# Performance work log

Hardware: AMD Instinct MI355X
Metric: run time of the kernel (lower is better)

## Reference

```python
import jax, jax.numpy as jnp
import numpy as np

N_NODES = 100000
N_EDGES = 1600000
D = 128            # in_channels == hidden_channels
N_CLASSES = 10
N_GRAPHS = 512
N_CONVS = 3        # num_layers - 1


def _linear_params(key, d_in, d_out):
    kw, kb = jax.random.split(key)
    bound = 1.0 / np.sqrt(d_in)
    w = jax.random.uniform(kw, (d_in, d_out), jnp.float32, -bound, bound)
    b = jax.random.uniform(kb, (d_out,), jnp.float32, -bound, bound)
    return w, b


def setup_inputs() -> dict:
    key = jax.random.key(0)
    ks = jax.random.split(key, 16)
    x = jax.random.normal(ks[0], (N_NODES, D), jnp.float32)
    edge_index = jax.random.randint(ks[1], (2, N_EDGES), 0, N_NODES, jnp.int64)
    batch = jnp.sort(jax.random.randint(ks[2], (N_NODES,), 0, N_GRAPHS, jnp.int64))
    inp = {"x": x, "edge_index": edge_index, "batch": batch}
    # 3 GIN convs, each an MLP: Linear(D,D) -> ReLU -> Linear(D,D)
    for i in range(N_CONVS):
        w1, b1 = _linear_params(ks[3 + 2 * i], D, D)
        w2, b2 = _linear_params(ks[4 + 2 * i], D, D)
        inp[f"w1_{i}"], inp[f"b1_{i}"] = w1, b1
        inp[f"w2_{i}"], inp[f"b2_{i}"] = w2, b2
    wl, bl = _linear_params(ks[10], D, N_CLASSES)
    inp["w_lin"], inp["b_lin"] = wl, bl
    return inp


def _gin_conv(x, src, dst, w1, b1, w2, b2):
    # sum_{j->i} x_j  (scatter-add over edges), eps = 0 (PyG default)
    agg = jax.ops.segment_sum(x[src], dst, num_segments=N_NODES)
    h = agg + x  # (1 + eps) * x + aggregate
    h = jax.nn.relu(h @ w1 + b1) @ w2 + b2  # nn.Sequential MLP
    return h


def reference(x, edge_index, batch,
              w1_0, b1_0, w2_0, b2_0,
              w1_1, b1_1, w2_1, b2_1,
              w1_2, b1_2, w2_2, b2_2,
              w_lin, b_lin):
    src, dst = edge_index[0], edge_index[1]
    params = [(w1_0, b1_0, w2_0, b2_0),
              (w1_1, b1_1, w2_1, b2_1),
              (w1_2, b1_2, w2_2, b2_2)]
    for (w1, b1, w2, b2) in params:
        x = _gin_conv(x, src, dst, w1, b1, w2, b2)
        x = jax.nn.relu(x)
    pooled = jax.ops.segment_sum(x, batch, num_segments=N_GRAPHS)  # global_add_pool
    return pooled @ w_lin + b_lin
```

## Files before the change

### kernel.cpp

```cpp
#include <hip/hip_runtime.h>
#include <hip/hip_bf16.h>

#define N_NODES 100000
#define N_EDGES 1600000
#define DIM 128
#define N_GRAPHS 512
#define N_CLASSES 10
#define SCAN_CHUNK 1024

#define NBK 782
#define EB 8192
#define NEB 196
#define HN (NBK * NEB)
#define NCH_HIST ((HN + SCAN_CHUNK - 1) / SCAN_CHUNK)

#define POOL_CHUNK 128
#define NPB ((N_NODES + POOL_CHUNK - 1) / POOL_CHUNK)

typedef __attribute__((ext_vector_type(8))) short short8;
typedef __attribute__((ext_vector_type(4))) float floatx4;

__device__ __forceinline__ uint bfround(float f) {
    uint u = __builtin_bit_cast(uint, f);
    return (u + 0x7fffu + ((u >> 16) & 1u)) >> 16;
}
__device__ __forceinline__ float bflo(uint u) { return __builtin_bit_cast(float, u << 16); }
__device__ __forceinline__ float bfhi(uint u) { return __builtin_bit_cast(float, u & 0xffff0000u); }

__device__ __forceinline__ void addrow(float* a, uint4 v) {
    a[0] += bflo(v.x); a[1] += bfhi(v.x);
    a[2] += bflo(v.y); a[3] += bfhi(v.y);
    a[4] += bflo(v.z); a[5] += bfhi(v.z);
    a[6] += bflo(v.w); a[7] += bfhi(v.w);
}

struct WPtrs { const float* w[6]; };

__global__ void k_cvt_x(const float* __restrict__ x, ushort* __restrict__ xb,
                        WPtrs wp, ushort* __restrict__ wt) {
    int stride = gridDim.x * blockDim.x;
    int t0 = blockIdx.x * blockDim.x + threadIdx.x;
    for (int i = t0; i < N_NODES * DIM / 4; i += stride) {
        floatx4 v = *(const floatx4*)(x + (size_t)i * 4);
        ushort4 o;
        o.x = (ushort)bfround(v.x);
        o.y = (ushort)bfround(v.y);
        o.z = (ushort)bfround(v.z);
        o.w = (ushort)bfround(v.w);
        *(ushort4*)(xb + (size_t)i * 4) = o;
    }
    for (int j = t0; j < 6 * 16384; j += stride) {
        int m = j >> 14, idx = j & 16383;
        int n = idx >> 7, k = idx & 127;
        wt[j] = (ushort)bfround(wp.w[m][k * 128 + n]);
    }
}


__global__ __launch_bounds__(256) void k_hist(const int* __restrict__ dstv,
                                              int* __restrict__ hist,
                                              float* __restrict__ pooled) {
    int gt = blockIdx.x * 256 + threadIdx.x;
    for (int i = gt; i < N_GRAPHS * DIM; i += NEB * 256) pooled[i] = 0.f;

    __shared__ int cnt[NBK];
    int blk = blockIdx.x, tid = threadIdx.x;
    for (int i = tid; i < NBK; i += 256) cnt[i] = 0;
    __syncthreads();
    int base = blk * EB;
    int end = min(base + EB, N_EDGES);
    for (int i = base + tid; i < end; i += 256) atomicAdd(&cnt[dstv[i] >> 7], 1);
    __syncthreads();
    for (int b = tid; b < NBK; b += 256) hist[b * NEB + blk] = cnt[b];
}

__global__ __launch_bounds__(256) void k_reduce(const int* __restrict__ src, int n,
                                                int* __restrict__ chunk_sums) {
    int base = blockIdx.x * SCAN_CHUNK;
    int tid = threadIdx.x;
    int s = 0;
    for (int i = tid; i < SCAN_CHUNK; i += 256) {
        int idx = base + i;
        if (idx < n) s += src[idx];
    }
    __shared__ int red[256];
    red[tid] = s;
    __syncthreads();
    for (int off = 128; off > 0; off >>= 1) {
        if (tid < off) red[tid] += red[tid + off];
        __syncthreads();
    }
    if (tid == 0) chunk_sums[blockIdx.x] = red[0];
}

__global__ __launch_bounds__(256) void k_scan_c(int* __restrict__ chunk_sums, int nch) {
    __shared__ int sm[256];
    int tid = threadIdx.x;
    int v = (tid < nch) ? chunk_sums[tid] : 0;
    sm[tid] = v;
    __syncthreads();
    for (int off = 1; off < 256; off <<= 1) {
        int t = (tid >= off) ? sm[tid - off] : 0;
        __syncthreads();
        sm[tid] += t;
        __syncthreads();
    }
    if (tid < nch) chunk_sums[tid] = sm[tid] - v;
}

__global__ __launch_bounds__(256) void k_apply(const int* __restrict__ src,
                                               const int* __restrict__ chunk_sums,
                                               int* __restrict__ dst, int n) {
    int base = blockIdx.x * SCAN_CHUNK;
    int tid = threadIdx.x;
    int i0 = base + tid * 4;
    int v[4];
    int s = 0;
    #pragma unroll
    for (int j = 0; j < 4; j++) {
        int idx = i0 + j;
        v[j] = (idx < n) ? src[idx] : 0;
        s += v[j];
    }
    __shared__ int sc[256];
    sc[tid] = s;
    __syncthreads();
    for (int off = 1; off < 256; off <<= 1) {
        int t = (tid >= off) ? sc[tid - off] : 0;
        __syncthreads();
        sc[tid] += t;
        __syncthreads();
    }
    int excl = sc[tid] - s + chunk_sums[blockIdx.x];
    #pragma unroll
    for (int j = 0; j < 4; j++) {
        int idx = i0 + j;
        if (idx < n) dst[idx] = excl;
        excl += v[j];
    }
}

__global__ __launch_bounds__(256) void k_scatter(const int* __restrict__ srcv,
                                                 const int* __restrict__ dstv,
                                                 const int* __restrict__ hists,
                                                 uint* __restrict__ sorted) {
    __shared__ int cur[NBK];
    int blk = blockIdx.x, tid = threadIdx.x;
    for (int b = tid; b < NBK; b += 256) cur[b] = hists[b * NEB + blk];
    __syncthreads();
    int base = blk * EB;
    int end = min(base + EB, N_EDGES);
    for (int i = base + tid; i < end; i += 256) {
        int s = srcv[i], d = dstv[i];
        int p = atomicAdd(&cur[d >> 7], 1);
        sorted[p] = (uint)s | ((uint)(d & 127) << 17);
    }
}

__global__ __launch_bounds__(256) void k_build(const int* __restrict__ hists,
                                               const uint* __restrict__ sorted,
                                               int* __restrict__ row_ptr,
                                               int* __restrict__ col) {
    __shared__ int cnt[128];
    __shared__ int scn[128];
    __shared__ int cur[128];
    int b = blockIdx.x, tid = threadIdx.x;
    if (tid < 128) cnt[tid] = 0;
    __syncthreads();
    int s0 = hists[b * NEB];
    int s1 = (b == NBK - 1) ? N_EDGES : hists[(b + 1) * NEB];
    for (int i = s0 + tid; i < s1; i += 256) atomicAdd(&cnt[(sorted[i] >> 17) & 127], 1);
    __syncthreads();
    if (tid < 128) scn[tid] = cnt[tid];
    __syncthreads();
    for (int off = 1; off < 128; off <<= 1) {
        int t = (tid < 128 && tid >= off) ? scn[tid - off] : 0;
        __syncthreads();
        if (tid < 128) scn[tid] += t;
        __syncthreads();
    }
    int node = (b << 7) + tid;
    if (tid < 128) {
        int excl = s0 + scn[tid] - cnt[tid];
        cur[tid] = excl;
        if (node < N_NODES) row_ptr[node] = excl;
    }
    if (b == 0 && tid == 0) row_ptr[N_NODES] = N_EDGES;
    __syncthreads();
    for (int i = s0 + tid; i < s1; i += 256) {
        uint e = sorted[i];
        int p = atomicAdd(&cur[(e >> 17) & 127], 1);
        col[p] = (int)(e & 0x1FFFFu);
    }
}

__global__ __launch_bounds__(256) void k_agg(const uint4* __restrict__ xr,
                                             const int* __restrict__ row_ptr,
                                             const int* __restrict__ col,
                                             uint4* __restrict__ hr) {
    int wv = threadIdx.x >> 6;
    int nA = blockIdx.x * 8 + wv * 2;
    if (nA >= N_NODES) return;
    int nB = nA + 1;
    bool hasB = nB < N_NODES;
    int lane = threadIdx.x & 63;
    int grp = lane >> 4;
    int l16 = lane & 15;

    float accA[8], accB[8];
    #pragma unroll
    for (int i = 0; i < 8; i++) { accA[i] = 0.f; accB[i] = 0.f; }
    if (grp == 0) {
        uint4 sv = xr[(size_t)nA * 16 + l16];
        accA[0] = bflo(sv.x); accA[1] = bfhi(sv.x);
        accA[2] = bflo(sv.y); accA[3] = bfhi(sv.y);
        accA[4] = bflo(sv.z); accA[5] = bfhi(sv.z);
        accA[6] = bflo(sv.w); accA[7] = bfhi(sv.w);
    } else if (grp == 1 && hasB) {
        uint4 sv = xr[(size_t)nB * 16 + l16];
        accB[0] = bflo(sv.x); accB[1] = bfhi(sv.x);
        accB[2] = bflo(sv.y); accB[3] = bfhi(sv.y);
        accB[4] = bflo(sv.z); accB[5] = bfhi(sv.z);
        accB[6] = bflo(sv.w); accB[7] = bfhi(sv.w);
    }

    int jA = row_ptr[nA], eA = row_ptr[nA + 1];
    int jB = hasB ? row_ptr[nB] : 0;
    int eB = hasB ? row_ptr[nB + 1] : 0;

    while (jA < eA || jB < eB) {
        int chunkA = eA - jA; chunkA = chunkA < 0 ? 0 : (chunkA > 64 ? 64 : chunkA);
        int chunkB = eB - jB; chunkB = chunkB < 0 ? 0 : (chunkB > 64 ? 64 : chunkB);
        int myA = (lane < chunkA) ? col[jA + lane] : 0;
        int myB = (lane < chunkB) ? col[jB + lane] : 0;
        int cm = chunkA > chunkB ? chunkA : chunkB;
        int iters = (cm + 15) >> 4;
        for (int f = 0; f < iters; f++) {
            int p = (f << 4) + grp;
            int a0 = __shfl(myA, (p      < chunkA) ? p      : 0);
            int a1 = __shfl(myA, (p + 4  < chunkA) ? p + 4  : 0);
            int a2 = __shfl(myA, (p + 8  < chunkA) ? p + 8  : 0);
            int a3 = __shfl(myA, (p + 12 < chunkA) ? p + 12 : 0);
            int b0 = __shfl(myB, (p      < chunkB) ? p      : 0);
            int b1 = __shfl(myB, (p + 4  < chunkB) ? p + 4  : 0);
            int b2 = __shfl(myB, (p + 8  < chunkB) ? p + 8  : 0);
            int b3 = __shfl(myB, (p + 12 < chunkB) ? p + 12 : 0);
            uint4 vA0 = xr[(size_t)a0 * 16 + l16];
            uint4 vA1 = xr[(size_t)a1 * 16 + l16];
            uint4 vA2 = xr[(size_t)a2 * 16 + l16];
            uint4 vA3 = xr[(size_t)a3 * 16 + l16];
            uint4 vB0 = xr[(size_t)b0 * 16 + l16];
            uint4 vB1 = xr[(size_t)b1 * 16 + l16];
            uint4 vB2 = xr[(size_t)b2 * 16 + l16];
            uint4 vB3 = xr[(size_t)b3 * 16 + l16];
            if (p < chunkA)      addrow(accA, vA0);
            if (p + 4 < chunkA)  addrow(accA, vA1);
            if (p + 8 < chunkA)  addrow(accA, vA2);
            if (p + 12 < chunkA) addrow(accA, vA3);
            if (p < chunkB)      addrow(accB, vB0);
            if (p + 4 < chunkB)  addrow(accB, vB1);
            if (p + 8 < chunkB)  addrow(accB, vB2);
            if (p + 12 < chunkB) addrow(accB, vB3);
        }
        jA += 64; jB += 64;
    }

    #pragma unroll
    for (int i = 0; i < 8; i++) {
        accA[i] += __shfl_xor(accA[i], 16);
        accA[i] += __shfl_xor(accA[i], 32);
        accB[i] += __shfl_xor(accB[i], 16);
        accB[i] += __shfl_xor(accB[i], 32);
    }

    if (grp == 0) {
        uint4 o;
        o.x = bfround(accA[0]) | (bfround(accA[1]) << 16);
        o.y = bfround(accA[2]) | (bfround(accA[3]) << 16);
        o.z = bfround(accA[4]) | (bfround(accA[5]) << 16);
        o.w = bfround(accA[6]) | (bfround(accA[7]) << 16);
        hr[(size_t)nA * 16 + l16] = o;
    } else if (grp == 1 && hasB) {
        uint4 o;
        o.x = bfround(accB[0]) | (bfround(accB[1]) << 16);
        o.y = bfround(accB[2]) | (bfround(accB[3]) << 16);
        o.z = bfround(accB[4]) | (bfround(accB[5]) << 16);
        o.w = bfround(accB[6]) | (bfround(accB[7]) << 16);
        hr[(size_t)nB * 16 + l16] = o;
    }
}

__device__ __forceinline__ int loff(int row, int byte) {
    return row * 256 + (byte ^ ((row & 7) << 4));
}

__global__ __launch_bounds__(256) void k_mlp(const ushort* __restrict__ hin,
                                             ushort* __restrict__ xout,
                                             const ushort* __restrict__ W1t,
                                             const float* __restrict__ b1,
                                             const ushort* __restrict__ W2t,
                                             const float* __restrict__ b2) {
    __shared__ alignas(16) char hT[64 * 256];
    int tid = threadIdx.x;
    int lane = tid & 63;
    int wave = tid >> 6;
    int node0 = blockIdx.x * 64;
    int l15 = lane & 15;
    int lhi = lane >> 4;
    int ncol0 = wave * 32;

    #pragma unroll
    for (int it = 0; it < 4; ++it) {
        int idx = it * 256 + tid;
        int row = idx >> 4;
        int cb = (idx & 15) * 16;
        int gn = node0 + row;
        floatx4 v = {0.f, 0.f, 0.f, 0.f};
        if (gn < N_NODES) v = *(const floatx4*)(hin + (size_t)gn * 128 + cb / 2);
        *(floatx4*)(hT + loff(row, cb)) = v;
    }
    __syncthreads();

    short8 bf[4][2];
    #pragma unroll
    for (int ks = 0; ks < 4; ks++)
        #pragma unroll
        for (int nf = 0; nf < 2; nf++) {
            int nrow = ncol0 + nf * 16 + l15;
            bf[ks][nf] = *(const short8*)(W1t + nrow * 128 + ks * 32 + lhi * 8);
        }

    floatx4 acc[4][2];
    #pragma unroll
    for (int m = 0; m < 4; m++)
        #pragma unroll
        for (int nf = 0; nf < 2; nf++) {
            float bias = b1[ncol0 + nf * 16 + l15];
            acc[m][nf] = (floatx4){bias, bias, bias, bias};
        }

    #pragma unroll
    for (int ks = 0; ks < 4; ks++) {
        short8 af[4];
        #pragma unroll
        for (int m = 0; m < 4; m++)
            af[m] = *(const short8*)(hT + loff(m * 16 + l15, ks * 64 + lhi * 16));
        #pragma unroll
        for (int m = 0; m < 4; m++)
            #pragma unroll
            for (int nf = 0; nf < 2; nf++)
                acc[m][nf] = __builtin_amdgcn_mfma_f32_16x16x32_bf16(af[m], bf[ks][nf], acc[m][nf], 0, 0, 0);
    }
    __syncthreads();

    #pragma unroll
    for (int m = 0; m < 4; m++)
        #pragma unroll
        for (int nf = 0; nf < 2; nf++) {
            int colb = (ncol0 + nf * 16 + l15) * 2;
            #pragma unroll
            for (int j = 0; j < 4; j++) {
                int row = m * 16 + lhi * 4 + j;
                float t = acc[m][nf][j];
                t = t > 0.f ? t : 0.f;
                *(ushort*)(hT + loff(row, colb)) = (ushort)bfround(t);
            }
        }
    __syncthreads();

    #pragma unroll
    for (int ks = 0; ks < 4; ks++)
        #pragma unroll
        for (int nf = 0; nf < 2; nf++) {
            int nrow = ncol0 + nf * 16 + l15;
            bf[ks][nf] = *(const short8*)(W2t + nrow * 128 + ks * 32 + lhi * 8);
        }
    #pragma unroll
    for (int m = 0; m < 4; m++)
        #pragma unroll
        for (int nf = 0; nf < 2; nf++) {
            float bias = b2[ncol0 + nf * 16 + l15];
            acc[m][nf] = (floatx4){bias, bias, bias, bias};
        }

    #pragma unroll
    for (int ks = 0; ks < 4; ks++) {
        short8 af[4];
        #pragma unroll
        for (int m = 0; m < 4; m++)
            af[m] = *(const short8*)(hT + loff(m * 16 + l15, ks * 64 + lhi * 16));
        #pragma unroll
        for (int m = 0; m < 4; m++)
            #pragma unroll
            for (int nf = 0; nf < 2; nf++)
                acc[m][nf] = __builtin_amdgcn_mfma_f32_16x16x32_bf16(af[m], bf[ks][nf], acc[m][nf], 0, 0, 0);
    }
    __syncthreads();

    #pragma unroll
    for (int m = 0; m < 4; m++)
        #pragma unroll
        for (int nf = 0; nf < 2; nf++) {
            int colb = (ncol0 + nf * 16 + l15) * 2;
            #pragma unroll
            for (int j = 0; j < 4; j++) {
                int row = m * 16 + lhi * 4 + j;
                float t = acc[m][nf][j];
                t = t > 0.f ? t : 0.f;
                *(ushort*)(hT + loff(row, colb)) = (ushort)bfround(t);
            }
        }
    __syncthreads();
    #pragma unroll
    for (int it = 0; it < 4; ++it) {
        int idx = it * 256 + tid;
        int row = idx >> 4;
        int cb = (idx & 15) * 16;
        int gn = node0 + row;
        if (gn < N_NODES)
            *(floatx4*)(xout + (size_t)gn * 128 + cb / 2) = *(const floatx4*)(hT + loff(row, cb));
    }
}

__global__ __launch_bounds__(256) void k_pool(const uint* __restrict__ x,
                                              const int* __restrict__ batch,
                                              float* __restrict__ pooled) {
    int n0 = blockIdx.x * POOL_CHUNK;
    int wave = threadIdx.x >> 6;
    int lane = threadIdx.x & 63;
    float a0 = 0.f, a1 = 0.f;
    int cur = -1;
    int endn = min(n0 + POOL_CHUNK, N_NODES);
    for (int n = n0 + wave; n < endn; n += 4) {
        int g = batch[n];
        if (g != cur) {
            if (cur >= 0) {
                atomicAdd(&pooled[cur * 128 + lane * 2], a0);
                atomicAdd(&pooled[cur * 128 + lane * 2 + 1], a1);
            }
            cur = g; a0 = 0.f; a1 = 0.f;
        }
        uint v = x[(size_t)n * 64 + lane];
        a0 += bflo(v); a1 += bfhi(v);
    }
    if (cur >= 0) {
        atomicAdd(&pooled[cur * 128 + lane * 2], a0);
        atomicAdd(&pooled[cur * 128 + lane * 2 + 1], a1);
    }
}

__global__ __launch_bounds__(64) void k_final(const float* __restrict__ pooled,
                                              const float* __restrict__ wl,
                                              const float* __restrict__ bl,
                                              float* __restrict__ out) {
    int g = blockIdx.x;
    int o = threadIdx.x;
    if (o >= N_CLASSES) return;
    float acc = bl[o];
    for (int k = 0; k < 128; k++) acc += pooled[g * 128 + k] * wl[k * N_CLASSES + o];
    out[g * N_CLASSES + o] = acc;
}


extern "C" void kernel_launch(void* const* d_in, const int* in_sizes, int n_in,
                              void* d_out, int out_size, void* d_ws, size_t ws_size,
                              hipStream_t stream) {
    const float* x0  = (const float*)d_in[0];
    const int* ei    = (const int*)d_in[1];
    const int* batch = (const int*)d_in[2];
    const float* W1[3] = {(const float*)d_in[3], (const float*)d_in[7],  (const float*)d_in[11]};
    const float* B1[3] = {(const float*)d_in[4], (const float*)d_in[8],  (const float*)d_in[12]};
    const float* W2[3] = {(const float*)d_in[5], (const float*)d_in[9],  (const float*)d_in[13]};
    const float* B2[3] = {(const float*)d_in[6], (const float*)d_in[10], (const float*)d_in[14]};
    const float* wl = (const float*)d_in[15];
    const float* bl = (const float*)d_in[16];
    float* out = (float*)d_out;

    const int* srcv = ei;
    const int* dstv = ei + N_EDGES;

    char* w = (char*)d_ws;
    ushort* xb = (ushort*)w;
    ushort* hb = xb + (size_t)N_NODES * DIM;
    ushort* wt = hb + (size_t)N_NODES * DIM;
    float* pooled = (float*)(wt + 6 * 128 * 128);
    int* row_ptr = (int*)(pooled + N_GRAPHS * DIM);
    int* colidx  = row_ptr + (N_NODES + 2);
    int* chunk_sums = colidx + N_EDGES;
    int* hist    = chunk_sums + 256;
    uint* sorted = (uint*)(hist + HN + 1);

    WPtrs wp;
    wp.w[0] = W1[0]; wp.w[1] = W2[0]; wp.w[2] = W1[1];
    wp.w[3] = W2[1]; wp.w[4] = W1[2]; wp.w[5] = W2[2];
    hipLaunchKernelGGL(k_cvt_x, dim3(2048), dim3(256), 0, stream, x0, xb, wp, wt);

    hipLaunchKernelGGL(k_hist, dim3(NEB), dim3(256), 0, stream, dstv, hist, pooled);
    hipLaunchKernelGGL(k_reduce, dim3(NCH_HIST), dim3(256), 0, stream, hist, HN, chunk_sums);
    hipLaunchKernelGGL(k_scan_c, dim3(1), dim3(256), 0, stream, chunk_sums, NCH_HIST);
    hipLaunchKernelGGL(k_apply, dim3(NCH_HIST), dim3(256), 0, stream, hist, chunk_sums, hist, HN);
    hipLaunchKernelGGL(k_scatter, dim3(NEB), dim3(256), 0, stream, srcv, dstv, hist, sorted);
    hipLaunchKernelGGL(k_build, dim3(NBK), dim3(256), 0, stream, hist, sorted, row_ptr, colidx);

    dim3 aggGrid((N_NODES + 7) / 8), aggBlk(256);
    dim3 mlpGrid((N_NODES + 63) / 64), mlpBlk(256);
    for (int l = 0; l < 3; l++) {
        hipLaunchKernelGGL(k_agg, aggGrid, aggBlk, 0, stream,
                           (const uint4*)xb, row_ptr, colidx, (uint4*)hb);
        hipLaunchKernelGGL(k_mlp, mlpGrid, mlpBlk, 0, stream,
                           hb, xb, wt + (size_t)(2 * l) * 16384, B1[l],
                           wt + (size_t)(2 * l + 1) * 16384, B2[l]);
    }

    hipLaunchKernelGGL(k_pool, dim3(NPB), dim3(256), 0, stream, (const uint*)xb, batch, pooled);
    hipLaunchKernelGGL(k_final, dim3(N_GRAPHS), dim3(64), 0, stream, pooled, wl, bl, out);
}
```

Before: 330.6 us.

## Fuse conversion with histogram, fold chunk scan into apply, pool inside MLP

Merges the input/weight bf16 conversion kernel with the edge histogram kernel by splitting blocks by role. Removes the single-block chunk-scan kernel by having each apply block reduce the preceding chunk sums itself. Fuses global add pooling into the last MLP layer, reading results from shared memory instead of re-reading from global. This cuts three kernel launches and one pass over the node features, at the cost of redundant prefix reductions per block and extra atomics in the MLP kernel.

```diff
diff --git a/kernel.cpp b/kernel.cpp
--- a/kernel.cpp
+++ b/kernel.cpp
@@ -14,9 +14,6 @@
 #define HN (NBK * NEB)
 #define NCH_HIST ((HN + SCAN_CHUNK - 1) / SCAN_CHUNK)
 
-#define POOL_CHUNK 128
-#define NPB ((N_NODES + POOL_CHUNK - 1) / POOL_CHUNK)
-
 typedef __attribute__((ext_vector_type(8))) short short8;
 typedef __attribute__((ext_vector_type(4))) float floatx4;
 
@@ -36,42 +33,43 @@
 
 struct WPtrs { const float* w[6]; };
 
-__global__ void k_cvt_x(const float* __restrict__ x, ushort* __restrict__ xb,
-                        WPtrs wp, ushort* __restrict__ wt) {
-    int stride = gridDim.x * blockDim.x;
-    int t0 = blockIdx.x * blockDim.x + threadIdx.x;
-    for (int i = t0; i < N_NODES * DIM / 4; i += stride) {
-        floatx4 v = *(const floatx4*)(x + (size_t)i * 4);
-        ushort4 o;
-        o.x = (ushort)bfround(v.x);
-        o.y = (ushort)bfround(v.y);
-        o.z = (ushort)bfround(v.z);
-        o.w = (ushort)bfround(v.w);
-        *(ushort4*)(xb + (size_t)i * 4) = o;
-    }
-    for (int j = t0; j < 6 * 16384; j += stride) {
-        int m = j >> 14, idx = j & 16383;
-        int n = idx >> 7, k = idx & 127;
-        wt[j] = (ushort)bfround(wp.w[m][k * 128 + n]);
-    }
-}
-
-
-__global__ __launch_bounds__(256) void k_hist(const int* __restrict__ dstv,
-                                              int* __restrict__ hist,
-                                              float* __restrict__ pooled) {
-    int gt = blockIdx.x * 256 + threadIdx.x;
-    for (int i = gt; i < N_GRAPHS * DIM; i += NEB * 256) pooled[i] = 0.f;
-
+__global__ __launch_bounds__(256) void k_cvt_hist(const float* __restrict__ x,
+                                                  ushort* __restrict__ xb,
+                                                  WPtrs wp, ushort* __restrict__ wt,
+                                                  const int* __restrict__ dstv,
+                                                  int* __restrict__ hist,
+                                                  float* __restrict__ pooled) {
     __shared__ int cnt[NBK];
-    int blk = blockIdx.x, tid = threadIdx.x;
-    for (int i = tid; i < NBK; i += 256) cnt[i] = 0;
-    __syncthreads();
-    int base = blk * EB;
-    int end = min(base + EB, N_EDGES);
-    for (int i = base + tid; i < end; i += 256) atomicAdd(&cnt[dstv[i] >> 7], 1);
-    __syncthreads();
-    for (int b = tid; b < NBK; b += 256) hist[b * NEB + blk] = cnt[b];
+    int tid = threadIdx.x;
+    if (blockIdx.x < NEB) {
+        int blk = blockIdx.x;
+        int gt = blk * 256 + tid;
+        for (int i = gt; i < N_GRAPHS * DIM; i += NEB * 256) pooled[i] = 0.f;
+        for (int i = tid; i < NBK; i += 256) cnt[i] = 0;
+        __syncthreads();
+        int base = blk * EB;
+        int end = min(base + EB, N_EDGES);
+        for (int i = base + tid; i < end; i += 256) atomicAdd(&cnt[dstv[i] >> 7], 1);
+        __syncthreads();
+        for (int b = tid; b < NBK; b += 256) hist[b * NEB + blk] = cnt[b];
+    } else {
+        int stride = (gridDim.x - NEB) * 256;
+        int t0 = (blockIdx.x - NEB) * 256 + tid;
+        for (int i = t0; i < N_NODES * DIM / 4; i += stride) {
+            floatx4 v = *(const floatx4*)(x + (size_t)i * 4);
+            ushort4 o;
+            o.x = (ushort)bfround(v.x);
+            o.y = (ushort)bfround(v.y);
+            o.z = (ushort)bfround(v.z);
+            o.w = (ushort)bfround(v.w);
+            *(ushort4*)(xb + (size_t)i * 4) = o;
+        }
+        for (int j = t0; j < 6 * 16384; j += stride) {
+            int m = j >> 14, idx = j & 16383;
+            int n = idx >> 7, k = idx & 127;
+            wt[j] = (ushort)bfround(wp.w[m][k * 128 + n]);
+        }
+    }
 }
 
 __global__ __launch_bounds__(256) void k_reduce(const int* __restrict__ src, int n,
@@ -93,26 +91,23 @@
     if (tid == 0) chunk_sums[blockIdx.x] = red[0];
 }
 
-__global__ __launch_bounds__(256) void k_scan_c(int* __restrict__ chunk_sums, int nch) {
-    __shared__ int sm[256];
-    int tid = threadIdx.x;
-    int v = (tid < nch) ? chunk_sums[tid] : 0;
-    sm[tid] = v;
-    __syncthreads();
-    for (int off = 1; off < 256; off <<= 1) {
-        int t = (tid >= off) ? sm[tid - off] : 0;
-        __syncthreads();
-        sm[tid] += t;
-        __syncthreads();
-    }
-    if (tid < nch) chunk_sums[tid] = sm[tid] - v;
-}
-
 __global__ __launch_bounds__(256) void k_apply(const int* __restrict__ src,
                                                const int* __restrict__ chunk_sums,
+                                               int nch,
                                                int* __restrict__ dst, int n) {
+    int tid = threadIdx.x;
+    __shared__ int red[256];
+    int ps = (tid < blockIdx.x && tid < nch) ? chunk_sums[tid] : 0;
+    red[tid] = ps;
+    __syncthreads();
+    for (int off = 128; off > 0; off >>= 1) {
+        if (tid < off) red[tid] += red[tid + off];
+        __syncthreads();
+    }
+    int prefix = red[0];
+    __syncthreads();
+
     int base = blockIdx.x * SCAN_CHUNK;
-    int tid = threadIdx.x;
     int i0 = base + tid * 4;
     int v[4];
     int s = 0;
@@ -131,7 +126,7 @@
         sc[tid] += t;
         __syncthreads();
     }
-    int excl = sc[tid] - s + chunk_sums[blockIdx.x];
+    int excl = sc[tid] - s + prefix;
     #pragma unroll
     for (int j = 0; j < 4; j++) {
         int idx = i0 + j;
@@ -299,7 +294,10 @@
                                              const ushort* __restrict__ W1t,
                                              const float* __restrict__ b1,
                                              const ushort* __restrict__ W2t,
-                                             const float* __restrict__ b2) {
+                                             const float* __restrict__ b2,
+                                             const int* __restrict__ batch,
+                                             float* __restrict__ pooled,
+                                             int dopool) {
     __shared__ alignas(16) char hT[64 * 256];
     int tid = threadIdx.x;
     int lane = tid & 63;
@@ -420,32 +418,29 @@
         if (gn < N_NODES)
             *(floatx4*)(xout + (size_t)gn * 128 + cb / 2) = *(const floatx4*)(hT + loff(row, cb));
     }
-}
-
-__global__ __launch_bounds__(256) void k_pool(const uint* __restrict__ x,
-                                              const int* __restrict__ batch,
-                                              float* __restrict__ pooled) {
-    int n0 = blockIdx.x * POOL_CHUNK;
-    int wave = threadIdx.x >> 6;
-    int lane = threadIdx.x & 63;
-    float a0 = 0.f, a1 = 0.f;
-    int cur = -1;
-    int endn = min(n0 + POOL_CHUNK, N_NODES);
-    for (int n = n0 + wave; n < endn; n += 4) {
-        int g = batch[n];
-        if (g != cur) {
-            if (cur >= 0) {
-                atomicAdd(&pooled[cur * 128 + lane * 2], a0);
-                atomicAdd(&pooled[cur * 128 + lane * 2 + 1], a1);
+
+    if (dopool) {
+        float a0 = 0.f, a1 = 0.f;
+        int cur = -1;
+        for (int i = 0; i < 16; i++) {
+            int row = wave * 16 + i;
+            int gn = node0 + row;
+            if (gn >= N_NODES) break;
+            int g = batch[gn];
+            if (g != cur) {
+                if (cur >= 0) {
+                    atomicAdd(&pooled[cur * 128 + lane * 2], a0);
+                    atomicAdd(&pooled[cur * 128 + lane * 2 + 1], a1);
+                }
+                cur = g; a0 = 0.f; a1 = 0.f;
             }
-            cur = g; a0 = 0.f; a1 = 0.f;
-        }
-        uint v = x[(size_t)n * 64 + lane];
-        a0 += bflo(v); a1 += bfhi(v);
-    }
-    if (cur >= 0) {
-        atomicAdd(&pooled[cur * 128 + lane * 2], a0);
-        atomicAdd(&pooled[cur * 128 + lane * 2 + 1], a1);
+            uint v = *(const uint*)(hT + loff(row, lane * 4));
+            a0 += bflo(v); a1 += bfhi(v);
+        }
+        if (cur >= 0) {
+            atomicAdd(&pooled[cur * 128 + lane * 2], a0);
+            atomicAdd(&pooled[cur * 128 + lane * 2 + 1], a1);
+        }
     }
 }
 
@@ -493,12 +488,12 @@
     WPtrs wp;
     wp.w[0] = W1[0]; wp.w[1] = W2[0]; wp.w[2] = W1[1];
     wp.w[3] = W2[1]; wp.w[4] = W1[2]; wp.w[5] = W2[2];
-    hipLaunchKernelGGL(k_cvt_x, dim3(2048), dim3(256), 0, stream, x0, xb, wp, wt);
-
-    hipLaunchKernelGGL(k_hist, dim3(NEB), dim3(256), 0, stream, dstv, hist, pooled);
+    hipLaunchKernelGGL(k_cvt_hist, dim3(2048 + NEB), dim3(256), 0, stream,
+                       x0, xb, wp, wt, dstv, hist, pooled);
+
     hipLaunchKernelGGL(k_reduce, dim3(NCH_HIST), dim3(256), 0, stream, hist, HN, chunk_sums);
-    hipLaunchKernelGGL(k_scan_c, dim3(1), dim3(256), 0, stream, chunk_sums, NCH_HIST);
-    hipLaunchKernelGGL(k_apply, dim3(NCH_HIST), dim3(256), 0, stream, hist, chunk_sums, hist, HN);
+    hipLaunchKernelGGL(k_apply, dim3(NCH_HIST), dim3(256), 0, stream,
+                       hist, chunk_sums, NCH_HIST, hist, HN);
     hipLaunchKernelGGL(k_scatter, dim3(NEB), dim3(256), 0, stream, srcv, dstv, hist, sorted);
     hipLaunchKernelGGL(k_build, dim3(NBK), dim3(256), 0, stream, hist, sorted, row_ptr, colidx);
 
@@ -509,9 +504,9 @@
                            (const uint4*)xb, row_ptr, colidx, (uint4*)hb);
         hipLaunchKernelGGL(k_mlp, mlpGrid, mlpBlk, 0, stream,
                            hb, xb, wt + (size_t)(2 * l) * 16384, B1[l],
-                           wt + (size_t)(2 * l + 1) * 16384, B2[l]);
-    }
-
-    hipLaunchKernelGGL(k_pool, dim3(NPB), dim3(256), 0, stream, (const uint*)xb, batch, pooled);
+                           wt + (size_t)(2 * l + 1) * 16384, B2[l],
+                           batch, pooled, (l == 2) ? 1 : 0);
+    }
+
     hipLaunchKernelGGL(k_final, dim3(N_GRAPHS), dim3(64), 0, stream, pooled, wl, bl, out);
 }
```

After: 314.2 us. 5.0% less time.
